# Kernel optimization log

Hardware: AMD Instinct MI355X
Metric: run time of the kernel (lower is better)

## Reference

```python
import jax, jax.numpy as jnp
import numpy as np

H = 16       # num_attention_heads
DH = 64      # attention_head_size
D = H * DH   # hidden_size = 1024
SCALE = DH ** -0.5


def setup_inputs() -> dict:
    key = jax.random.key(0)
    ks = jax.random.split(key, 9)
    s = 0.02
    return {
        "hidden_states": jax.random.normal(ks[0], (2, 2048, D), jnp.float32),
        "Wq": jax.random.normal(ks[1], (D, D), jnp.float32) * s,
        "bq": jax.random.normal(ks[2], (D,), jnp.float32) * s,
        "Wk": jax.random.normal(ks[3], (D, D), jnp.float32) * s,
        "bk": jax.random.normal(ks[4], (D,), jnp.float32) * s,
        "Wv": jax.random.normal(ks[5], (D, D), jnp.float32) * s,
        "bv": jax.random.normal(ks[6], (D,), jnp.float32) * s,
        "Wo": jax.random.normal(ks[7], (D, D), jnp.float32) * s,
        "bo": jax.random.normal(ks[8], (D,), jnp.float32) * s,
    }


def reference(hidden_states, Wq, bq, Wk, bk, Wv, bv, Wo, bo):
    B, S, _ = hidden_states.shape
    # project and split into heads: [B, H, S, DH]
    def heads(x):
        return x.reshape(B, S, H, DH).transpose(0, 2, 1, 3)
    q = heads(hidden_states @ Wq + bq)
    k = heads(hidden_states @ Wk + bk)
    v = heads(hidden_states @ Wv + bv)
    # eager attention: full [B,H,S,S] scores, softmax in fp32
    scores = jnp.einsum("bhqd,bhkd->bhqk", q, k) * SCALE
    probs = jax.nn.softmax(scores.astype(jnp.float32), axis=-1).astype(q.dtype)
    ctx = jnp.einsum("bhqk,bhkd->bqhd", probs, v).reshape(B, S, D)
    # output projection (dropout inactive at eval)
    return ctx @ Wo + bo
```

## Files before the change

kernel.cpp:

```cpp
#include <hip/hip_runtime.h>

typedef __bf16 bf16;
typedef __bf16 bf16x8 __attribute__((ext_vector_type(8)));
typedef __bf16 bf16x4 __attribute__((ext_vector_type(4)));
typedef __bf16 bf16x2 __attribute__((ext_vector_type(2)));
typedef float  f32x4  __attribute__((ext_vector_type(4)));
typedef unsigned u32x2 __attribute__((ext_vector_type(2)));
typedef unsigned u32x4 __attribute__((ext_vector_type(4)));

#define DEV __device__ __forceinline__

DEV int detect_f32(const void* x) {
  const unsigned short* u = (const unsigned short*)x;
  int lane = threadIdx.x & 63;
  int e = (u[lane * 8] >> 7) & 0xFF;
  unsigned long long b = __ballot(e >= 118 && e <= 134);
  return __popcll(b) < 32;
}

DEV void gl2lds16(const bf16* g, bf16* l) {
  __builtin_amdgcn_global_load_lds(
      (const __attribute__((address_space(1))) void*)g,
      (__attribute__((address_space(3))) void*)l, 16, 0, 0);
}

DEV unsigned pack_bf16(float a, float b) {
  bf16x2 t;
  t[0] = (bf16)a;
  t[1] = (bf16)b;
  return __builtin_bit_cast(unsigned, t);
}

__global__ __launch_bounds__(256) void prep(
    const void* __restrict__ X, const void* __restrict__ bq,
    const void* __restrict__ bk, const void* __restrict__ bv,
    const void* __restrict__ bo, const void* __restrict__ Wq,
    const void* __restrict__ Wk, const void* __restrict__ Wv,
    const void* __restrict__ Wo, bf16* __restrict__ Xb,
    bf16* __restrict__ bqkv, bf16* __restrict__ bob,
    bf16* __restrict__ Wtqkv, bf16* __restrict__ Wto) {
  __shared__ __align__(16) bf16 T[64 * 80];
  int f32 = detect_f32(X);
  int blk = blockIdx.x, tid = threadIdx.x;
  if (blk < 2048) {
    long base = (long)blk * 2048 + tid * 8;
    bf16x8 o;
    if (f32) {
      const float* s = (const float*)X + base;
#pragma unroll
      for (int i = 0; i < 8; ++i) o[i] = (bf16)s[i];
    } else {
      o = *(const bf16x8*)((const bf16*)X + base);
    }
    *(bf16x8*)&Xb[base] = o;
  } else if (blk < 2052) {
    const void* src = (blk == 2048) ? bq : (blk == 2049) ? bk : (blk == 2050) ? bv : bo;
    bf16* dst = (blk == 2051) ? bob : bqkv + (blk - 2048) * 1024;
    int base = tid * 4;
    if (f32) {
      const float* s = (const float*)src;
#pragma unroll
      for (int i = 0; i < 4; ++i) dst[base + i] = (bf16)s[base + i];
    } else {
      const bf16* s = (const bf16*)src;
#pragma unroll
      for (int i = 0; i < 4; ++i) dst[base + i] = s[base + i];
    }
  } else {
    int id = blk - 2052;
    int z = id >> 8, r = id & 255;
    int k0 = (r & 15) * 64, n0 = (r >> 4) * 64;
    const void* src = (z == 0) ? Wq : (z == 1) ? Wk : (z == 2) ? Wv : Wo;
    bf16* dst = (z < 3) ? (Wtqkv + (long)z * 1048576) : Wto;
#pragma unroll
    for (int c = 0; c < 2; ++c) {
      int lin = tid + c * 256;
      int row = lin >> 3, col8 = (lin & 7) * 8;
      long gidx = (long)(k0 + row) * 1024 + n0 + col8;
      bf16x8 v;
      if (f32) {
        const float* s = (const float*)src + gidx;
#pragma unroll
        for (int i = 0; i < 8; ++i) v[i] = (bf16)s[i];
      } else {
        v = *(const bf16x8*)((const bf16*)src + gidx);
      }
      *(bf16x8*)&T[row * 80 + col8] = v;
    }
    __syncthreads();
#pragma unroll
    for (int c = 0; c < 2; ++c) {
      int lin = tid + c * 256;
      int row = lin >> 3, col8 = (lin & 7) * 8;
      bf16x8 v;
#pragma unroll
      for (int i = 0; i < 8; ++i) v[i] = T[(col8 + i) * 80 + row];
      *(bf16x8*)&dst[(long)(n0 + row) * 1024 + k0 + col8] = v;
    }
  }
}

template <int TM, int TN, int MODE>
__global__ __launch_bounds__(256, 3) void gemm_bt(
    const bf16* __restrict__ A, const bf16* __restrict__ Bt, int M, int N,
    int K, void* __restrict__ Cout, const bf16* __restrict__ bias,
    const void* __restrict__ detect_src, bf16* __restrict__ Qo,
    bf16* __restrict__ Ko, bf16* __restrict__ Vo) {
  constexpr int NWN = TN / 64;
  constexpr int NWM = 4 / NWN;
  constexpr int MT = TM / (NWM * 16);
  __shared__ __align__(16) bf16 GS[TM * 64 + TN * 64];
  bf16* As = GS;
  bf16* Bs = GS + TM * 64;
  int tid = threadIdx.x, lane = tid & 63, wave = tid >> 6;
  int quad = lane >> 4, l16 = lane & 15;
  int lin = blockIdx.x + blockIdx.y * gridDim.x;
  int cpx = (gridDim.x * gridDim.y) >> 3;
  int swz = (lin & 7) * cpx + (lin >> 3);
  int bx = swz % gridDim.x, by = swz / gridDim.x;
  int m0 = bx * TM, n0 = by * TN;
  int wm = (wave / NWN) * (TM / NWM), wn = (wave % NWN) * 64;
  f32x4 zero = {0.f, 0.f, 0.f, 0.f};
  f32x4 acc[MT][4];
#pragma unroll
  for (int i = 0; i < MT; ++i)
#pragma unroll
    for (int j = 0; j < 4; ++j) acc[i][j] = zero;

  for (int k0 = 0; k0 < K; k0 += 64) {
#pragma unroll
    for (int i = 0; i < TM / 32; ++i) {
      int u = (i * 4 + wave) * 64 + lane;
      int r = u >> 3, g = (u & 7) ^ (r & 7);
      gl2lds16(A + (long)(m0 + r) * K + k0 + g * 8, As + (i * 4 + wave) * 512);
    }
#pragma unroll
    for (int i = 0; i < TN / 32; ++i) {
      int u = (i * 4 + wave) * 64 + lane;
      int r = u >> 3, g = (u & 7) ^ (r & 7);
      gl2lds16(Bt + (long)(n0 + r) * K + k0 + g * 8, Bs + (i * 4 + wave) * 512);
    }
    __syncthreads();
#pragma unroll
    for (int kc = 0; kc < 2; ++kc) {
      bf16x8 bv_[4];
#pragma unroll
      for (int nt = 0; nt < 4; ++nt) {
        int row = wn + nt * 16 + l16;
        bv_[nt] = *(const bf16x8*)&Bs[row * 64 + (((kc * 4 + quad) ^ (l16 & 7))) * 8];
      }
#pragma unroll
      for (int mt = 0; mt < MT; ++mt) {
        int row = wm + mt * 16 + l16;
        bf16x8 af = *(const bf16x8*)&As[row * 64 + (((kc * 4 + quad) ^ (l16 & 7))) * 8];
#pragma unroll
        for (int nt = 0; nt < 4; ++nt)
          acc[mt][nt] = __builtin_amdgcn_mfma_f32_16x16x32_bf16(bv_[nt], af,
                                                                acc[mt][nt], 0, 0, 0);
      }
    }
    __syncthreads();
  }

  if (MODE == 0) {
    int f32o = detect_f32(detect_src);
#pragma unroll
    for (int nt = 0; nt < 4; ++nt) {
      int n = n0 + wn + nt * 16 + quad * 4;
      bf16x4 bb = *(const bf16x4*)&bias[n];
#pragma unroll
      for (int mt = 0; mt < MT; ++mt) {
        int m = m0 + wm + mt * 16 + l16;
        if (f32o) {
          f32x4 v;
#pragma unroll
          for (int r = 0; r < 4; ++r) v[r] = acc[mt][nt][r] + (float)bb[r];
          *(f32x4*)((float*)Cout + (long)m * N + n) = v;
        } else {
          bf16x4 v;
#pragma unroll
          for (int r = 0; r < 4; ++r) v[r] = (bf16)(acc[mt][nt][r] + (float)bb[r]);
          *(bf16x4*)((bf16*)Cout + (long)m * N + n) = v;
        }
      }
    }
  } else {
    int t = n0 >> 10;
    if (t < 2) {
      float qsc = (t == 0) ? 0.1803368801f : 1.0f;
      bf16* op = (t == 0) ? Qo : Ko;
#pragma unroll
      for (int nt = 0; nt < 4; ++nt) {
        int n = n0 + wn + nt * 16 + quad * 4;
        bf16x4 bb = *(const bf16x4*)&bias[n];
        int nl = n & 1023, h = nl >> 6, dh = nl & 63;
#pragma unroll
        for (int mt = 0; mt < MT; ++mt) {
          int m = m0 + wm + mt * 16 + l16;
          int b = m >> 11, s = m & 2047;
          bf16x4 v;
#pragma unroll
          for (int r = 0; r < 4; ++r)
            v[r] = (bf16)((acc[mt][nt][r] + (float)bb[r]) * qsc);
          *(bf16x4*)&op[((long)(b * 16 + h) * 2048 + s) * 64 + dh] = v;
        }
      }
    } else {
      bf16* T = GS;
#pragma unroll
      for (int nt = 0; nt < 4; ++nt) {
        int n = wn + nt * 16 + quad * 4;
        bf16x4 bb = *(const bf16x4*)&bias[n0 + n];
#pragma unroll
        for (int mt = 0; mt < MT; ++mt) {
          int m = wm + mt * 16 + l16;
#pragma unroll
          for (int r = 0; r < 4; ++r)
            T[(n + r) * 128 + m] = (bf16)(acc[mt][nt][r] + (float)bb[r]);
        }
      }
      __syncthreads();
      int b = m0 >> 11, s0 = m0 & 2047;
      int h0 = (n0 & 1023) >> 6;
#pragma unroll
      for (int c = 0; c < 8; ++c) {
        int u = c * 256 + tid;
        int row = u >> 4, col = (u & 15) * 8;
        bf16x8 v = *(const bf16x8*)&T[row * 128 + col];
        long base =
            ((long)(b * 16 + h0 + (row >> 6)) * 64 + (row & 63)) * 2048 + s0;
        *(bf16x8*)&Vo[base + col] = v;
      }
    }
  }
}

__global__ __launch_bounds__(512, 4) void attn(const bf16* __restrict__ Qg,
                                               const bf16* __restrict__ Kg,
                                               const bf16* __restrict__ Vtg,
                                               bf16* __restrict__ ctx) {
  __shared__ __align__(16) bf16 SMEM[32768];
  bf16* Ksh = SMEM;
  bf16* Vsh = SMEM + 16384;
  float* MG = (float*)SMEM;

  int tid = threadIdx.x, lane = tid & 63, w = tid >> 6;
  int grp = w >> 2, wq = w & 3;
  int quad = lane >> 4, l16 = lane & 15;
  int lin = blockIdx.x | (blockIdx.y << 4);
  int swz = ((lin & 7) << 6) | (lin >> 3);
  int bh = swz >> 4, q0 = (swz & 15) << 7;
  const bf16* Qh = Qg + (long)bh * 131072;
  const bf16* Kh = Kg + (long)bh * 131072;
  const bf16* Vh = Vtg + (long)bh * 131072;
  int qbase = q0 + wq * 32;

  bf16x8 qf[2][2];
#pragma unroll
  for (int nt = 0; nt < 2; ++nt)
#pragma unroll
    for (int kc = 0; kc < 2; ++kc)
      qf[nt][kc] = *(const bf16x8*)&Qh[(long)(qbase + nt * 16 + l16) * 64 +
                                       kc * 32 + quad * 8];

  int e0 = l16 * 64 + (quad ^ (l16 & 7)) * 8;
  int e1 = l16 * 64 + ((4 + quad) ^ (l16 & 7)) * 8;

  int mS = tid >> 3, gS = (tid & 7) ^ (mS & 7);
  int kvpS = (mS & 32) + ((mS & 12) << 1) + ((mS & 16) >> 2) + (mS & 3);
  int koff = kvpS * 64 + gS * 8;
  int voff = mS * 2048 + gS * 8;
  int ldsoff = tid * 8;

  auto stage1 = [&](int t) {
    int buf = t & 3;
    gl2lds16(Kh + (long)t * 4096 + koff, Ksh + buf * 4096 + ldsoff);
    gl2lds16(Vh + t * 64 + voff, Vsh + buf * 4096 + ldsoff);
  };

  bf16x8 onesv;
#pragma unroll
  for (int i = 0; i < 8; ++i) onesv[i] = (bf16)1.0f;

  f32x4 zero = {0.f, 0.f, 0.f, 0.f};
  f32x4 O[2][4];
  f32x4 Ol[2] = {zero, zero};
#pragma unroll
  for (int i = 0; i < 2; ++i)
#pragma unroll
    for (int j = 0; j < 4; ++j) O[i][j] = zero;

  auto compute = [&](const bf16* Kb, const bf16* Vb) {
    u32x2 pk[4][2];
#pragma unroll
    for (int mt = 0; mt < 4; ++mt) {
      bf16x8 kf0 = *(const bf16x8*)&Kb[e0 + mt * 1024];
      bf16x8 kf1 = *(const bf16x8*)&Kb[e1 + mt * 1024];
#pragma unroll
      for (int nt = 0; nt < 2; ++nt) {
        f32x4 s_ = zero;
        __builtin_amdgcn_s_setprio(1);
        s_ = __builtin_amdgcn_mfma_f32_16x16x32_bf16(kf0, qf[nt][0], s_, 0, 0, 0);
        s_ = __builtin_amdgcn_mfma_f32_16x16x32_bf16(kf1, qf[nt][1], s_, 0, 0, 0);
        __builtin_amdgcn_s_setprio(0);
        f32x4 p;
        p[0] = __builtin_amdgcn_exp2f(s_[0]);
        p[1] = __builtin_amdgcn_exp2f(s_[1]);
        p[2] = __builtin_amdgcn_exp2f(s_[2]);
        p[3] = __builtin_amdgcn_exp2f(s_[3]);
        pk[mt][nt][0] = pack_bf16(p[0], p[1]);
        pk[mt][nt][1] = pack_bf16(p[2], p[3]);
      }
    }
#pragma unroll
    for (int c = 0; c < 2; ++c) {
      bf16x8 pb[2];
#pragma unroll
      for (int nt = 0; nt < 2; ++nt) {
        u32x4 tt;
        tt[0] = pk[2 * c][nt][0];
        tt[1] = pk[2 * c][nt][1];
        tt[2] = pk[2 * c + 1][nt][0];
        tt[3] = pk[2 * c + 1][nt][1];
        pb[nt] = __builtin_bit_cast(bf16x8, tt);
      }
      int ec = c ? e1 : e0;
      __builtin_amdgcn_s_setprio(1);
#pragma unroll
      for (int dt = 0; dt < 4; ++dt) {
        bf16x8 vf = *(const bf16x8*)&Vb[ec + dt * 1024];
#pragma unroll
        for (int nt = 0; nt < 2; ++nt)
          O[nt][dt] = __builtin_amdgcn_mfma_f32_16x16x32_bf16(vf, pb[nt],
                                                              O[nt][dt], 0, 0, 0);
      }
#pragma unroll
      for (int nt = 0; nt < 2; ++nt)
        Ol[nt] = __builtin_amdgcn_mfma_f32_16x16x32_bf16(onesv, pb[nt],
                                                         Ol[nt], 0, 0, 0);
      __builtin_amdgcn_s_setprio(0);
    }
  };

  stage1(0);
  stage1(1);
  for (int it = 0; it < 16; ++it) {
    __syncthreads();
    int ta = 2 * it + 2;
    if (ta < 32) {
      stage1(ta);
      stage1(ta + 1);
    }
    int t = 2 * it + grp;
    compute(Ksh + (t & 3) * 4096, Vsh + (t & 3) * 4096);
  }

  float lsum[2] = {Ol[0][0], Ol[1][0]};

  __syncthreads();
  float* Mp = MG + wq * 2176;
  if (grp == 1) {
#pragma unroll
    for (int nt = 0; nt < 2; ++nt) {
#pragma unroll
      for (int dt = 0; dt < 4; ++dt)
        *(f32x4*)&Mp[((nt * 4 + dt) * 64 + lane) * 4] = O[nt][dt];
      Mp[2048 + nt * 64 + lane] = lsum[nt];
    }
  }
  __syncthreads();
  if (grp == 0) {
#pragma unroll
    for (int nt = 0; nt < 2; ++nt) {
#pragma unroll
      for (int dt = 0; dt < 4; ++dt) {
        f32x4 o2 = *(const f32x4*)&Mp[((nt * 4 + dt) * 64 + lane) * 4];
#pragma unroll
        for (int r = 0; r < 4; ++r) O[nt][dt][r] += o2[r];
      }
      lsum[nt] += Mp[2048 + nt * 64 + lane];
    }
    float rv[2];
#pragma unroll
    for (int nt = 0; nt < 2; ++nt) rv[nt] = __builtin_amdgcn_rcpf(lsum[nt]);
    int b = bh >> 4, h = bh & 15;
#pragma unroll
    for (int nt = 0; nt < 2; ++nt) {
      int s = qbase + nt * 16 + l16;
#pragma unroll
      for (int dt = 0; dt < 4; ++dt) {
        bf16x4 v;
#pragma unroll
        for (int r = 0; r < 4; ++r) v[r] = (bf16)(O[nt][dt][r] * rv[nt]);
        *(bf16x4*)&ctx[((long)(b * 2048 + s)) * 1024 + h * 64 + dt * 16 +
                       quad * 4] = v;
      }
    }
  }
}

extern "C" void kernel_launch(void* const* d_in, const int* in_sizes, int n_in,
                              void* d_out, int out_size, void* d_ws,
                              size_t ws_size, hipStream_t stream) {
  const void* X  = d_in[0];
  const void* Wq = d_in[1]; const void* bq = d_in[2];
  const void* Wk = d_in[3]; const void* bk = d_in[4];
  const void* Wv = d_in[5]; const void* bv = d_in[6];
  const void* Wo = d_in[7]; const void* bo = d_in[8];

  char* ws = (char*)d_ws;
  bf16* Xb    = (bf16*)(ws);
  bf16* Wtqkv = (bf16*)(ws + 8388608);
  bf16* Wto   = (bf16*)(ws + 14680064);
  bf16* bqkv  = (bf16*)(ws + 16777216);
  bf16* bob   = (bf16*)(ws + 16783360);
  bf16* Qw    = (bf16*)(ws + 16785408);
  bf16* Kw    = (bf16*)(ws + 25174016);
  bf16* Cx    = (bf16*)(ws + 33562624);
  bf16* Vt    = (bf16*)(ws + 41951232);

  prep<<<dim3(3076), 256, 0, stream>>>(X, bq, bk, bv, bo, Wq, Wk, Wv, Wo, Xb,
                                       bqkv, bob, Wtqkv, Wto);
  gemm_bt<128, 128, 1><<<dim3(32, 24), 256, 0, stream>>>(
      Xb, Wtqkv, 4096, 3072, 1024, nullptr, bqkv, nullptr, Qw, Kw, Vt);
  attn<<<dim3(16, 32), 512, 0, stream>>>(Qw, Kw, Vt, Cx);
  gemm_bt<128, 64, 0><<<dim3(32, 16), 256, 0, stream>>>(
      Cx, Wto, 4096, 1024, 1024, d_out, bob, X, nullptr, nullptr, nullptr);
}
```

Baseline: 178.0 us.

## Software-pipeline QK and PV across tiles with six-slot V buffer

Splits the per-tile attention compute into separate QK/exp and PV phases and interleaves them so each tile's PV runs after the next tile's QK. The goal is to overlap MFMA work with the exp/pack dependency chain. V gets a six-slot LDS ring so a tile's V stays resident across the extra iteration, which grows shared memory from 64KB to 80KB. That growth may lower occupancy, and holding two sets of packed probabilities raises register pressure. The first PV call runs on zeroed probabilities as a no-op warm-up.

New measurement: 178.9 us. Within noise of the previous version (+0.5%).

```diff
diff --git a/kernel.cpp b/kernel.cpp
--- a/kernel.cpp
+++ b/kernel.cpp
@@ -239,7 +239,7 @@
                                                const bf16* __restrict__ Kg,
                                                const bf16* __restrict__ Vtg,
                                                bf16* __restrict__ ctx) {
-  __shared__ __align__(16) bf16 SMEM[32768];
+  __shared__ __align__(16) bf16 SMEM[40960];
   bf16* Ksh = SMEM;
   bf16* Vsh = SMEM + 16384;
   float* MG = (float*)SMEM;
@@ -273,9 +273,8 @@
   int ldsoff = tid * 8;
 
   auto stage1 = [&](int t) {
-    int buf = t & 3;
-    gl2lds16(Kh + (long)t * 4096 + koff, Ksh + buf * 4096 + ldsoff);
-    gl2lds16(Vh + t * 64 + voff, Vsh + buf * 4096 + ldsoff);
+    gl2lds16(Kh + (long)t * 4096 + koff, Ksh + (t & 3) * 4096 + ldsoff);
+    gl2lds16(Vh + t * 64 + voff, Vsh + (t % 6) * 4096 + ldsoff);
   };
 
   bf16x8 onesv;
@@ -290,8 +289,7 @@
 #pragma unroll
     for (int j = 0; j < 4; ++j) O[i][j] = zero;
 
-  auto compute = [&](const bf16* Kb, const bf16* Vb) {
-    u32x2 pk[4][2];
+  auto qk = [&](const bf16* Kb, u32x2 (&pk)[4][2]) {
 #pragma unroll
     for (int mt = 0; mt < 4; ++mt) {
       bf16x8 kf0 = *(const bf16x8*)&Kb[e0 + mt * 1024];
@@ -312,6 +310,9 @@
         pk[mt][nt][1] = pack_bf16(p[2], p[3]);
       }
     }
+  };
+
+  auto pv = [&](const bf16* Vb, u32x2 (&pk)[4][2]) {
 #pragma unroll
     for (int c = 0; c < 2; ++c) {
       bf16x8 pb[2];
@@ -342,18 +343,38 @@
     }
   };
 
+  u32x2 pkA[4][2], pkB[4][2];
+#pragma unroll
+  for (int i = 0; i < 4; ++i)
+#pragma unroll
+    for (int j = 0; j < 2; ++j) {
+      u32x2 z2 = {0u, 0u};
+      pkB[i][j] = z2;
+    }
+
   stage1(0);
   stage1(1);
-  for (int it = 0; it < 16; ++it) {
+  int vbA = 0, vbB = 0;
+  for (int it2 = 0; it2 < 8; ++it2) {
+    int tA = 4 * it2 + grp, tB = tA + 2;
     __syncthreads();
-    int ta = 2 * it + 2;
-    if (ta < 32) {
-      stage1(ta);
-      stage1(ta + 1);
-    }
-    int t = 2 * it + grp;
-    compute(Ksh + (t & 3) * 4096, Vsh + (t & 3) * 4096);
-  }
+    {
+      int ta = 4 * it2 + 2;
+      if (ta < 32) { stage1(ta); stage1(ta + 1); }
+    }
+    pv(Vsh + vbB, pkB);
+    qk(Ksh + (tA & 3) * 4096, pkA);
+    vbA = (tA % 6) * 4096;
+    __syncthreads();
+    {
+      int ta = 4 * it2 + 4;
+      if (ta < 32) { stage1(ta); stage1(ta + 1); }
+    }
+    pv(Vsh + vbA, pkA);
+    qk(Ksh + (tB & 3) * 4096, pkB);
+    vbB = (tB % 6) * 4096;
+  }
+  pv(Vsh + vbB, pkB);
 
   float lsum[2] = {Ol[0][0], Ol[1][0]};
 
```
